# Kernel optimization log

Measured on AMD Instinct MI355X. Metric: run time of the kernel, lower is better.

## Reference

```python
import jax, jax.numpy as jnp
import numpy as np

D_MODEL = 2048
NUM_HEADS = 16
D_HEAD = D_MODEL // NUM_HEADS


def setup_inputs() -> dict:
    key = jax.random.key(0)
    k_x, k_q, k_k, k_v, k_o, k_ob = jax.random.split(key, 6)
    B, L = 2, 2048
    s = 1.0 / np.sqrt(D_MODEL)
    return {
        "x": jax.random.normal(k_x, (B, L, D_MODEL), dtype=jnp.float32),
        # torch nn.Linear weights are (out_features, in_features)
        "Wq": jax.random.uniform(k_q, (D_MODEL, D_MODEL), jnp.float32, -s, s),
        "Wk": jax.random.uniform(k_k, (D_HEAD, D_MODEL), jnp.float32, -s, s),
        "Wv": jax.random.uniform(k_v, (D_HEAD, D_MODEL), jnp.float32, -s, s),
        "Wo": jax.random.uniform(k_o, (D_MODEL, D_MODEL), jnp.float32, -s, s),
        "bo": jax.random.uniform(k_ob, (D_MODEL,), jnp.float32, -s, s),
    }


def reference(x, Wq, Wk, Wv, Wo, bo):
    B, L, _ = x.shape
    H, dh = NUM_HEADS, D_HEAD
    Q = (x @ Wq.T).reshape(B, L, H, dh).transpose(0, 2, 1, 3)  # [B,H,L,dh]
    K = x @ Wk.T  # [B,L,dh] shared across heads (MQA)
    V = x @ Wv.T  # [B,L,dh]
    scores = jnp.einsum("bhqd,bkd->bhqk", Q, K) / np.sqrt(dh)  # [B,H,L,L]
    attn = jax.nn.softmax(scores, axis=-1)
    out = jnp.einsum("bhqk,bkd->bhqd", attn, V)  # [B,H,L,dh]
    out = out.transpose(0, 2, 1, 3).reshape(B, L, H * dh)
    return out @ Wo.T + bo
```

## Files before the change

kernel.cpp:

```cpp
#include <hip/hip_runtime.h>


typedef __attribute__((ext_vector_type(8))) short bf16x8;
typedef __attribute__((ext_vector_type(4))) short short4v;
typedef __attribute__((ext_vector_type(4))) float f32x4;
typedef __attribute__((ext_vector_type(16))) float f32x16;
typedef __attribute__((ext_vector_type(4))) int int4v;

__device__ __forceinline__ unsigned short f2bf(float f) {
  unsigned int u = __builtin_bit_cast(unsigned int, f);
  u += 0x7fffu + ((u >> 16) & 1u);
  return (unsigned short)(u >> 16);
}

__device__ __forceinline__ unsigned int cvtpk(float lo, float hi) {
  unsigned int r;
  asm("v_cvt_pk_bf16_f32 %0, %1, %2" : "=v"(r) : "v"(lo), "v"(hi));
  return r;
}

typedef __attribute__((address_space(1))) void gvoid_t;
typedef __attribute__((address_space(3))) void lvoid_t;

__device__ __forceinline__ void gll16(const void* g, void* l) {
  __builtin_amdgcn_global_load_lds((gvoid_t*)g, (lvoid_t*)l, 16, 0, 0);
}

__global__ void cast_all_kernel(
    const float* __restrict__ x, const float* __restrict__ wq,
    const float* __restrict__ wk, const float* __restrict__ wv,
    const float* __restrict__ wo, unsigned short* __restrict__ xb,
    unsigned short* __restrict__ wallb, unsigned short* __restrict__ wob) {
  const int NT = 4325376;
  int i = blockIdx.x * blockDim.x + threadIdx.x;
  const int stride = gridDim.x * blockDim.x;
  for (; i < NT; i += stride) {
    const float* src;
    unsigned short* dst;
    int j;
    if (i < 2097152) {
      src = x; dst = xb; j = i;
    } else if (i < 3145728) {
      src = wq; dst = wallb; j = i - 2097152;
    } else if (i < 3211264) {
      src = wk; dst = wallb + 2048 * 2048; j = i - 3145728;
    } else if (i < 3276800) {
      src = wv; dst = wallb + 2176 * 2048; j = i - 3211264;
    } else {
      src = wo; dst = wob; j = i - 3276800;
    }
    float4 f = reinterpret_cast<const float4*>(src)[j];
    short4v o;
    o.x = (short)f2bf(f.x);
    o.y = (short)f2bf(f.y);
    o.z = (short)f2bf(f.z);
    o.w = (short)f2bf(f.w);
    reinterpret_cast<short4v*>(dst)[j] = o;
  }
}

template <int MODE>
__global__ __launch_bounds__(256) void gemm_bt(
    const unsigned short* __restrict__ A, const unsigned short* __restrict__ B,
    void* __restrict__ Cout, int M, int N, int K, float scale,
    const float* __restrict__ bias, void* __restrict__ C2,
    void* __restrict__ C3) {
  __shared__ unsigned short As[128 * 32] __attribute__((aligned(16)));
  __shared__ unsigned short Bs[128 * 32] __attribute__((aligned(16)));

  const int tid = threadIdx.x;
  const int lane = tid & 63;
  const int wave = tid >> 6;
  const int lr = lane & 15;
  const int lg = lane >> 4;
  const int nwgx = gridDim.x;
  const int l = blockIdx.y * nwgx + blockIdx.x;
  const int qc = (nwgx * gridDim.y) >> 3;
  const int s = (l & 7) * qc + (l >> 3);
  const int bm = (s % nwgx) * 128;
  const int bn = (s / nwgx) * 128;
  const int wrow = (wave >> 1) * 64;
  const int wcol = (wave & 1) * 64;

  f32x4 acc[4][4] = {};

  const int c0 = tid;
  const int c1 = tid + 256;

  for (int k0 = 0; k0 < K; k0 += 32) {
    __syncthreads();
    gll16(A + (size_t)(bm + (c0 >> 2)) * K + k0 + (c0 & 3) * 8,
          (char*)As + wave * 1024);
    gll16(A + (size_t)(bm + (c1 >> 2)) * K + k0 + (c1 & 3) * 8,
          (char*)As + 4096 + wave * 1024);
    gll16(B + (size_t)(bn + (c0 >> 2)) * K + k0 + (c0 & 3) * 8,
          (char*)Bs + wave * 1024);
    gll16(B + (size_t)(bn + (c1 >> 2)) * K + k0 + (c1 & 3) * 8,
          (char*)Bs + 4096 + wave * 1024);
    __syncthreads();

    bf16x8 af[4], bfr[4];
#pragma unroll
    for (int mi = 0; mi < 4; mi++)
      af[mi] = *(const bf16x8*)&As[(wrow + mi * 16 + lr) * 32 + 8 * lg];
#pragma unroll
    for (int nj = 0; nj < 4; nj++)
      bfr[nj] = *(const bf16x8*)&Bs[(wcol + nj * 16 + lr) * 32 + 8 * lg];
#pragma unroll
    for (int mi = 0; mi < 4; mi++)
#pragma unroll
      for (int nj = 0; nj < 4; nj++)
        acc[mi][nj] = __builtin_amdgcn_mfma_f32_16x16x32_bf16(
            af[mi], bfr[nj], acc[mi][nj], 0, 0, 0);
  }

#pragma unroll
  for (int mi = 0; mi < 4; mi++)
#pragma unroll
    for (int nj = 0; nj < 4; nj++) {
      const int row = bm + wrow + mi * 16 + lg * 4;
      const int col = bn + wcol + nj * 16 + lr;
#pragma unroll
      for (int r = 0; r < 4; r++) {
        float v = acc[mi][nj][r];
        if constexpr (MODE == 2) {
          ((float*)Cout)[(size_t)(row + r) * N + col] = v + bias[col];
        } else {
          if (col < 2048)
            ((unsigned short*)Cout)[(size_t)(row + r) * 2048 + col] =
                f2bf(v * scale);
          else if (col < 2176)
            ((unsigned short*)C2)[(size_t)(row + r) * 128 + (col - 2048)] =
                f2bf(v);
          else
            ((unsigned short*)C3)[(size_t)(col - 2176) * M + (row + r)] =
                f2bf(v);
        }
      }
    }
}

__global__ __launch_bounds__(256, 3) void mqa_attn(
    const unsigned short* __restrict__ Q, const unsigned short* __restrict__ Kb,
    const unsigned short* __restrict__ VT, unsigned short* __restrict__ Ob) {
  __shared__ unsigned short Ksm[2][2][4096] __attribute__((aligned(16)));
  __shared__ unsigned short Vsm[2][4096] __attribute__((aligned(16)));
  __shared__ float mlbuf[2][2][32];

  const int tid = threadIdx.x;
  const int lane = tid & 63;
  const int wave = tid >> 6;
  const int grp = wave >> 1;
  const int wi = wave & 1;
  const int tg = tid & 127;
  const int l31 = lane & 31;
  const int hi = lane >> 5;
  const int bh = blockIdx.y;
  const int b = bh >> 4;
  const int h = bh & 15;
  const int q0 = blockIdx.x * 64 + wi * 32;
  const int kvbase = grp * 1024;

  const unsigned short* Qb = Q + ((size_t)(b * 2048 + q0)) * 2048 + h * 128;
  const unsigned short* Kbase = Kb + (size_t)b * 2048 * 128;
  const unsigned short* VTb = VT + (size_t)b * 2048;

  bf16x8 qf[8];
#pragma unroll
  for (int ks = 0; ks < 8; ks++)
    qf[ks] = *(const bf16x8*)&Qb[(size_t)l31 * 2048 + ks * 16 + hi * 8];

  f32x16 oacc[4] = {};
  float mrun = -1e30f, lrun = 0.0f;

  int koff[4], voff[4];
#pragma unroll
  for (int t = 0; t < 4; t++) {
    int ci = t * 128 + tg;
    int row = ci >> 4;
    int p = (ci ^ row) & 15;
    koff[t] = row * 128 + p * 8;
    voff[t] = (4 * row + (p >> 2)) * 4096 + (p & 3) * 8;
  }

  auto stageK = [&](int kv0, int bsel) {
    const unsigned short* kp = Kbase + (size_t)(kvbase + kv0) * 128;
    char* kb = (char*)&Ksm[grp][bsel][0];
#pragma unroll
    for (int t = 0; t < 4; t++) gll16(kp + koff[t], kb + (t * 128 + tg) * 16);
  };
  auto stageV = [&](int kv0) {
    const unsigned short* vp = VTb + kvbase + kv0;
    char* vb = (char*)&Vsm[grp][0];
#pragma unroll
    for (int t = 0; t < 4; t++) gll16(vp + voff[t], vb + (t * 128 + tg) * 16);
  };

  stageK(0, 0);
  stageV(0);
  asm volatile("s_waitcnt vmcnt(0)" ::: "memory");
  __builtin_amdgcn_sched_barrier(0);
  __builtin_amdgcn_s_barrier();

  for (int t = 0; t < 32; t++) {
    const int cur = t & 1;
    stageK(((t + 1) & 31) * 32, cur ^ 1);
    const unsigned short* Kt = &Ksm[grp][cur][0];
    const unsigned short* Vt = &Vsm[grp][0];

    f32x16 st = {};
#pragma unroll
    for (int ks = 0; ks < 8; ks++) {
      const int pos = (2 * ks + hi) ^ (l31 & 15);
      bf16x8 kf = *(const bf16x8*)&Kt[l31 * 128 + pos * 8];
      st = __builtin_amdgcn_mfma_f32_32x32x16_bf16(kf, qf[ks], st, 0, 0, 0);
    }

    float u0 = fmaxf(fmaxf(st[0], st[1]), st[2]);
    float u1 = fmaxf(fmaxf(st[3], st[4]), st[5]);
    float u2 = fmaxf(fmaxf(st[6], st[7]), st[8]);
    float u3 = fmaxf(fmaxf(st[9], st[10]), st[11]);
    float u4 = fmaxf(fmaxf(st[12], st[13]), st[14]);
    float tm = fmaxf(fmaxf(fmaxf(u0, u1), u2), fmaxf(fmaxf(u3, u4), st[15]));
    tm = fmaxf(tm, __shfl_xor(tm, 32));

    if (!__all(tm <= mrun + 8.0f)) {
      float mnew = fmaxf(mrun, tm);
      float sc = __builtin_amdgcn_exp2f(mrun - mnew);
      mrun = mnew;
      lrun *= sc;
#pragma unroll
      for (int r = 0; r < 16; r++) {
        float scr = __shfl(sc, (r & 3) + 8 * (r >> 2) + 4 * hi);
#pragma unroll
        for (int dt = 0; dt < 4; dt++) oacc[dt][r] *= scr;
      }
    }

    float red[16];
#pragma unroll
    for (int r = 0; r < 16; r++) {
      st[r] = __builtin_amdgcn_exp2f(st[r] - mrun);
      red[r] = st[r];
    }
#pragma unroll
    for (int w = 8; w >= 1; w >>= 1)
#pragma unroll
      for (int r = 0; r < w; r++) red[r] += red[r + w];
    lrun += red[0] + __shfl_xor(red[0], 32);

    bf16x8 paw[2];
#pragma unroll
    for (int h2 = 0; h2 < 2; h2++) {
      unsigned int a0 = cvtpk(st[8 * h2 + 0], st[8 * h2 + 1]);
      unsigned int a1 = cvtpk(st[8 * h2 + 2], st[8 * h2 + 3]);
      unsigned int b0 = cvtpk(st[8 * h2 + 4], st[8 * h2 + 5]);
      unsigned int b1 = cvtpk(st[8 * h2 + 6], st[8 * h2 + 7]);
      unsigned int s0 = hi ? a0 : b0;
      unsigned int s1 = hi ? a1 : b1;
      unsigned int r0 = (unsigned int)__shfl_xor((int)s0, 32);
      unsigned int r1 = (unsigned int)__shfl_xor((int)s1, 32);
      int4v w;
      w.x = (int)(hi ? r0 : a0);
      w.y = (int)(hi ? r1 : a1);
      w.z = (int)(hi ? b0 : r0);
      w.w = (int)(hi ? b1 : r1);
      paw[h2] = __builtin_bit_cast(bf16x8, w);
    }

    asm volatile("s_waitcnt vmcnt(4)" ::: "memory");
    __builtin_amdgcn_sched_barrier(0);
    __builtin_amdgcn_s_barrier();

#pragma unroll
    for (int dt = 0; dt < 4; dt++) {
      f32x16 z = oacc[dt];
      const int qr = dt * 8 + (l31 >> 2);
#pragma unroll
      for (int ks2 = 0; ks2 < 2; ks2++) {
        const int pos = (4 * (l31 & 3) + 2 * ks2 + hi) ^ (qr & 15);
        bf16x8 vfr = *(const bf16x8*)&Vt[qr * 128 + pos * 8];
        z = __builtin_amdgcn_mfma_f32_32x32x16_bf16(paw[ks2], vfr, z, 0, 0, 0);
      }
      oacc[dt] = z;
    }

    __builtin_amdgcn_s_barrier();
    stageV(((t + 1) & 31) * 32);
    asm volatile("s_waitcnt vmcnt(4)" ::: "memory");
    __builtin_amdgcn_sched_barrier(0);
    __builtin_amdgcn_s_barrier();
  }

  float* mg = (float*)&Ksm[0][0][0] + (size_t)wi * 4096;
  if (grp == 1) {
#pragma unroll
    for (int dt = 0; dt < 4; dt++)
#pragma unroll
      for (int r = 0; r < 16; r++)
        mg[(dt * 16 + r) * 64 + lane] = oacc[dt][r];
    if (hi == 0) {
      mlbuf[wi][0][l31] = mrun;
      mlbuf[wi][1][l31] = lrun;
    }
  }
  __syncthreads();
  if (grp == 0) {
    float mb = mlbuf[wi][0][l31];
    float lb = mlbuf[wi][1][l31];
    float m = fmaxf(mrun, mb);
    float ca = __builtin_amdgcn_exp2f(mrun - m);
    float cb = __builtin_amdgcn_exp2f(mb - m);
    float linv = 1.0f / (lrun * ca + lb * cb);
    float wa = ca * linv, wb = cb * linv;
#pragma unroll
    for (int r = 0; r < 16; r++) {
      const int qrow = (r & 3) + 8 * (r >> 2) + 4 * hi;
      float war = __shfl(wa, qrow);
      float wbr = __shfl(wb, qrow);
      size_t row = (size_t)(b * 2048 + q0 + qrow);
#pragma unroll
      for (int dt = 0; dt < 4; dt++) {
        float o = oacc[dt][r] * war + mg[(dt * 16 + r) * 64 + lane] * wbr;
        Ob[row * 2048 + h * 128 + dt * 32 + l31] = f2bf(o);
      }
    }
  }
}

extern "C" void kernel_launch(void* const* d_in, const int* in_sizes, int n_in,
                              void* d_out, int out_size, void* d_ws,
                              size_t ws_size, hipStream_t stream) {
  const float* x = (const float*)d_in[0];
  const float* Wq = (const float*)d_in[1];
  const float* Wk = (const float*)d_in[2];
  const float* Wv = (const float*)d_in[3];
  const float* Wo = (const float*)d_in[4];
  const float* bo = (const float*)d_in[5];

  const int Bb = 2, Lq = 2048, D = 2048, DH = 128;
  const int M = Bb * Lq;

  char* ws = (char*)d_ws;
  size_t off = 0;
  auto alloc = [&](size_t bytes) {
    void* p = ws + off;
    off += (bytes + 255) & ~size_t(255);
    return p;
  };
  unsigned short* x_bf = (unsigned short*)alloc((size_t)M * D * 2);
  unsigned short* Wall_bf = (unsigned short*)alloc((size_t)2304 * D * 2);
  unsigned short* Wo_bf = (unsigned short*)alloc((size_t)D * D * 2);
  unsigned short* Qbuf = (unsigned short*)alloc((size_t)M * D * 2);
  unsigned short* Kbuf = (unsigned short*)alloc((size_t)M * DH * 2);
  unsigned short* VTbuf = (unsigned short*)alloc((size_t)DH * M * 2);
  unsigned short* AObuf = (unsigned short*)alloc((size_t)M * D * 2);

  cast_all_kernel<<<2048, 256, 0, stream>>>(x, Wq, Wk, Wv, Wo, x_bf, Wall_bf,
                                            Wo_bf);

  gemm_bt<4><<<dim3(M / 128, 2304 / 128), 256, 0, stream>>>(
      x_bf, Wall_bf, Qbuf, M, 2304, D, 0.12752041986f, nullptr, Kbuf, VTbuf);
  mqa_attn<<<dim3(Lq / 64, Bb * 16), 256, 0, stream>>>(Qbuf, Kbuf, VTbuf,
                                                       AObuf);
  gemm_bt<2><<<dim3(M / 128, D / 128), 256, 0, stream>>>(
      AObuf, Wo_bf, d_out, M, D, D, 1.0f, bo, nullptr, nullptr);
}
```

Baseline: 247.0 us.

## Double-buffer V tiles alongside K and drop GEMM tile swizzle

The attention kernel now keeps two V buffers, like K, and stages K and V for the next tile together at the top of each iteration. This removes two of the three per-iteration barriers and the separate V staging after the PV MFMAs, so V loads overlap with compute. The cost is 16KB more LDS, which may lower occupancy below the 3 blocks per CU set by the launch bounds. Separately, the GEMM drops its XCD-aware block remapping in favour of plain blockIdx mapping, which may change L2 locality.

```diff
diff --git a/kernel.cpp b/kernel.cpp
--- a/kernel.cpp
+++ b/kernel.cpp
@@ -73,12 +73,8 @@
   const int wave = tid >> 6;
   const int lr = lane & 15;
   const int lg = lane >> 4;
-  const int nwgx = gridDim.x;
-  const int l = blockIdx.y * nwgx + blockIdx.x;
-  const int qc = (nwgx * gridDim.y) >> 3;
-  const int s = (l & 7) * qc + (l >> 3);
-  const int bm = (s % nwgx) * 128;
-  const int bn = (s / nwgx) * 128;
+  const int bm = blockIdx.x * 128;
+  const int bn = blockIdx.y * 128;
   const int wrow = (wave >> 1) * 64;
   const int wcol = (wave & 1) * 64;
 
@@ -144,7 +140,7 @@
     const unsigned short* __restrict__ Q, const unsigned short* __restrict__ Kb,
     const unsigned short* __restrict__ VT, unsigned short* __restrict__ Ob) {
   __shared__ unsigned short Ksm[2][2][4096] __attribute__((aligned(16)));
-  __shared__ unsigned short Vsm[2][4096] __attribute__((aligned(16)));
+  __shared__ unsigned short Vsm[2][2][4096] __attribute__((aligned(16)));
   __shared__ float mlbuf[2][2][32];
 
   const int tid = threadIdx.x;
@@ -183,30 +179,28 @@
     voff[t] = (4 * row + (p >> 2)) * 4096 + (p & 3) * 8;
   }
 
-  auto stageK = [&](int kv0, int bsel) {
+  auto stage = [&](int kv0, int bsel) {
     const unsigned short* kp = Kbase + (size_t)(kvbase + kv0) * 128;
+    const unsigned short* vp = VTb + kvbase + kv0;
     char* kb = (char*)&Ksm[grp][bsel][0];
-#pragma unroll
-    for (int t = 0; t < 4; t++) gll16(kp + koff[t], kb + (t * 128 + tg) * 16);
+    char* vb = (char*)&Vsm[grp][bsel][0];
+#pragma unroll
+    for (int t = 0; t < 4; t++) {
+      gll16(kp + koff[t], kb + (t * 128 + tg) * 16);
+      gll16(vp + voff[t], vb + (t * 128 + tg) * 16);
+    }
   };
-  auto stageV = [&](int kv0) {
-    const unsigned short* vp = VTb + kvbase + kv0;
-    char* vb = (char*)&Vsm[grp][0];
-#pragma unroll
-    for (int t = 0; t < 4; t++) gll16(vp + voff[t], vb + (t * 128 + tg) * 16);
-  };
-
-  stageK(0, 0);
-  stageV(0);
+
+  stage(0, 0);
   asm volatile("s_waitcnt vmcnt(0)" ::: "memory");
   __builtin_amdgcn_sched_barrier(0);
   __builtin_amdgcn_s_barrier();
 
   for (int t = 0; t < 32; t++) {
     const int cur = t & 1;
-    stageK(((t + 1) & 31) * 32, cur ^ 1);
+    stage(((t + 1) & 31) * 32, cur ^ 1);
     const unsigned short* Kt = &Ksm[grp][cur][0];
-    const unsigned short* Vt = &Vsm[grp][0];
+    const unsigned short* Vt = &Vsm[grp][cur][0];
 
     f32x16 st = {};
 #pragma unroll
@@ -268,10 +262,6 @@
       paw[h2] = __builtin_bit_cast(bf16x8, w);
     }
 
-    asm volatile("s_waitcnt vmcnt(4)" ::: "memory");
-    __builtin_amdgcn_sched_barrier(0);
-    __builtin_amdgcn_s_barrier();
-
 #pragma unroll
     for (int dt = 0; dt < 4; dt++) {
       f32x16 z = oacc[dt];
@@ -285,9 +275,7 @@
       oacc[dt] = z;
     }
 
-    __builtin_amdgcn_s_barrier();
-    stageV(((t + 1) & 31) * 32);
-    asm volatile("s_waitcnt vmcnt(4)" ::: "memory");
+    asm volatile("s_waitcnt vmcnt(0)" ::: "memory");
     __builtin_amdgcn_sched_barrier(0);
     __builtin_amdgcn_s_barrier();
   }
```

Measured after the change: 306.3 us. +24.0%, slower.
